# Kernel tuning notes

Hardware: AMD Instinct MI355X
Metric: run time of the kernel (lower is better)

Reference implementation:

```python
import jax, jax.numpy as jnp
import numpy as np

V, BLK, C, H, L = 50257, 1024, 1024, 16, 4
B, T = 2, 1024
D = C // H
EPS = 1e-5

def _ln(x, w):
    mu = jnp.mean(x, axis=-1, keepdims=True)
    var = jnp.mean(jnp.square(x - mu), axis=-1, keepdims=True)
    return (x - mu) * jax.lax.rsqrt(var + EPS) * w

def setup_inputs() -> dict:
    key = jax.random.key(0)
    ks = jax.random.split(key, 9)
    s = 0.02
    return {
        'idx': jax.random.randint(ks[0], (B, T), 0, V),
        'wte': jax.random.normal(ks[1], (V, C), jnp.float32) * s,
        'wpe': jax.random.normal(ks[2], (BLK, C), jnp.float32) * s,
        'ln1_w': jnp.ones((L, C), jnp.float32),
        'attn_w': jax.random.normal(ks[3], (L, 3 * C, C), jnp.float32) * s,   # torch Linear [out,in]
        'attnproj_w': jax.random.normal(ks[4], (L, C, C), jnp.float32) * (s / np.sqrt(2 * L)),
        'ln2_w': jnp.ones((L, C), jnp.float32),
        'fc_w': jax.random.normal(ks[5], (L, 4 * C, C), jnp.float32) * s,
        'mlpproj_w': jax.random.normal(ks[6], (L, C, 4 * C), jnp.float32) * (s / np.sqrt(2 * L)),
        'lnf_w': jnp.ones((C,), jnp.float32),
        'head_w': jax.random.normal(ks[7], (V, C), jnp.float32) * s,
    }

def _block(x, ln1_w, attn_w, attnproj_w, ln2_w, fc_w, mlpproj_w):
    b, t, c = x.shape
    h = _ln(x, ln1_w)
    qkv = h @ attn_w.T                                  # [B,T,3C]
    q, k, v = jnp.split(qkv, 3, axis=-1)
    q = q.reshape(b, t, H, D).transpose(0, 2, 1, 3)      # [B,H,T,D]
    k = k.reshape(b, t, H, D).transpose(0, 2, 1, 3)
    v = v.reshape(b, t, H, D).transpose(0, 2, 1, 3)
    att = jnp.einsum('bhqd,bhkd->bhqk', q, k) * (1.0 / np.sqrt(D))
    causal = jnp.tril(jnp.ones((t, t), bool))
    att = jnp.where(causal, att, jnp.float32(-jnp.inf))
    p = jax.nn.softmax(att, axis=-1)
    y = jnp.einsum('bhqk,bhkd->bhqd', p, v)
    y = y.transpose(0, 2, 1, 3).reshape(b, t, c)
    y = y @ attnproj_w.T
    x = x + y
    m = _ln(x, ln2_w)
    m = jax.nn.relu(m @ fc_w.T) @ mlpproj_w.T
    return x + m

def reference(idx, wte, wpe, ln1_w, attn_w, attnproj_w, ln2_w, fc_w, mlpproj_w, lnf_w, head_w):
    t = idx.shape[1]
    x = wte[idx] + wpe[:t]                               # [B,T,C]
    for i in range(L):
        x = _block(x, ln1_w[i], attn_w[i], attnproj_w[i], ln2_w[i], fc_w[i], mlpproj_w[i])
    x = _ln(x, lnf_w)
    return x @ head_w.T                                  # logits [B,T,V]
```

## Files before the change

### kernel.cpp

```cpp
#include <hip/hip_runtime.h>

typedef __bf16 bf16x8 __attribute__((ext_vector_type(8)));
typedef float f32x4 __attribute__((ext_vector_type(4)));
typedef unsigned short u16x8 __attribute__((ext_vector_type(8)));

#define LOG2E 1.4426950408889634f

__device__ __forceinline__ unsigned short f2bf(float f) {
  union { float f; unsigned u; } v; v.f = f;
  return (unsigned short)((v.u + 0x7fffu + ((v.u >> 16) & 1u)) >> 16);
}

__device__ __forceinline__ void gload16(const void* g, void* l) {
  __builtin_amdgcn_global_load_lds(
      (const __attribute__((address_space(1))) unsigned int*)g,
      (__attribute__((address_space(3))) unsigned int*)l, 16, 0, 0);
}

__global__ __launch_bounds__(256) void cvt_kernel(
    const float* __restrict__ s, unsigned short* __restrict__ d, int n8) {
  int i = blockIdx.x * 256 + threadIdx.x;
  int stride = gridDim.x * 256;
  for (; i < n8; i += stride) {
    float4 a = ((const float4*)s)[2 * i];
    float4 b = ((const float4*)s)[2 * i + 1];
    u16x8 o;
    o[0] = f2bf(a.x); o[1] = f2bf(a.y); o[2] = f2bf(a.z); o[3] = f2bf(a.w);
    o[4] = f2bf(b.x); o[5] = f2bf(b.y); o[6] = f2bf(b.z); o[7] = f2bf(b.w);
    ((u16x8*)d)[i] = o;
  }
}

__global__ __launch_bounds__(256) void embed_kernel(
    const int* __restrict__ idx, const float* __restrict__ wte,
    const float* __restrict__ wpe, float* __restrict__ x) {
  int row = blockIdx.x;
  int tok = idx[row];
  int t = row & 1023;
  float4 a = ((const float4*)(wte + (size_t)tok * 1024))[threadIdx.x];
  float4 p = ((const float4*)(wpe + (size_t)t * 1024))[threadIdx.x];
  a.x += p.x; a.y += p.y; a.z += p.z; a.w += p.w;
  ((float4*)(x + (size_t)row * 1024))[threadIdx.x] = a;
}

__global__ __launch_bounds__(256) void ln_kernel(
    const float* __restrict__ x, const float* __restrict__ w,
    unsigned short* __restrict__ out) {
  __shared__ float2 red[4];
  int row = blockIdx.x, tid = threadIdx.x;
  float4 v = ((const float4*)(x + (size_t)row * 1024))[tid];
  float s  = v.x + v.y + v.z + v.w;
  float s2 = v.x * v.x + v.y * v.y + v.z * v.z + v.w * v.w;
#pragma unroll
  for (int m = 32; m >= 1; m >>= 1) {
    s  += __shfl_xor(s, m, 64);
    s2 += __shfl_xor(s2, m, 64);
  }
  if ((tid & 63) == 0) red[tid >> 6] = make_float2(s, s2);
  __syncthreads();
  float S = 0.f, S2 = 0.f;
#pragma unroll
  for (int i = 0; i < 4; ++i) { S += red[i].x; S2 += red[i].y; }
  float mu = S * (1.f / 1024.f);
  float var = S2 * (1.f / 1024.f) - mu * mu;
  float rs = rsqrtf(var + 1e-5f);
  float4 wv = ((const float4*)w)[tid];
  ushort4 o;
  o.x = f2bf((v.x - mu) * rs * wv.x);
  o.y = f2bf((v.y - mu) * rs * wv.y);
  o.z = f2bf((v.z - mu) * rs * wv.z);
  o.w = f2bf((v.w - mu) * rs * wv.w);
  ((ushort4*)(out + (size_t)row * 1024))[tid] = o;
}

template <int MODE, bool WB16>
__global__ __launch_bounds__(256, 2) void gemm_bt(
    const unsigned short* __restrict__ A, const void* __restrict__ Wp,
    void* __restrict__ outp, const float* __restrict__ resid,
    unsigned short* __restrict__ qo, unsigned short* __restrict__ ko,
    unsigned short* __restrict__ vo, int M, int N, int K) {
  __shared__ unsigned short As[2][128 * 64];
  __shared__ unsigned short Bs[2][128 * 64];

  const int tid = threadIdx.x;
  const int lane = tid & 63;
  const int wv = tid >> 6;
  const int lr = lane & 15, lh = lane >> 4;
  const int nbm = M >> 7;
  const int nb = gridDim.x;
  const int bid = blockIdx.x;
  const int swz = (bid & 7) * (nb >> 3) + (bid >> 3);
  const int m0 = (swz % nbm) << 7;
  const int n0 = (swz / nbm) << 7;
  const int wm = (wv >> 1) << 6;
  const int wn = (wv & 1) << 6;
  const int nK = K >> 6;

  float4 breg[8];
  const float* Wf = (const float*)Wp;
  const unsigned short* Wb = (const unsigned short*)Wp;

  auto loadB = [&](int kt) {
#pragma unroll
    for (int j = 0; j < 8; ++j) {
      int u = j * 256 + tid;
      int rn = n0 + (u >> 4);
      if (rn >= N) rn = N - 1;
      breg[j] = *(const float4*)(Wf + (size_t)rn * K + kt * 64 + (u & 15) * 4);
    }
  };
  auto writeB = [&](int buf) {
#pragma unroll
    for (int j = 0; j < 8; ++j) {
      int u = j * 256 + tid;
      int row = u >> 4, q = u & 15;
      ushort4 h4;
      h4.x = f2bf(breg[j].x); h4.y = f2bf(breg[j].y);
      h4.z = f2bf(breg[j].z); h4.w = f2bf(breg[j].w);
      int off = row * 128 + ((q * 8) ^ ((row & 7) << 4));
      *(ushort4*)((char*)(&Bs[buf][0]) + off) = h4;
    }
  };
  auto stageA = [&](int buf, int kt) {
    const unsigned short* base = A + (size_t)m0 * K + kt * 64;
#pragma unroll
    for (int j = 0; j < 4; ++j) {
      int u = j * 256 + tid;
      int row = u >> 3, un = u & 7;
      gload16(base + (size_t)row * K + ((un ^ (row & 7)) << 3),
              (char*)(&As[buf][0]) + u * 16);
    }
  };
  auto stageB16 = [&](int buf, int kt) {
#pragma unroll
    for (int j = 0; j < 4; ++j) {
      int u = j * 256 + tid;
      int row = u >> 3, un = u & 7;
      size_t grow = (size_t)(n0 + row);
      if constexpr (MODE == 4) { if ((int)grow >= N) grow = N - 1; }
      gload16(Wb + grow * K + kt * 64 + ((un ^ (row & 7)) << 3),
              (char*)(&Bs[buf][0]) + u * 16);
    }
  };

  f32x4 acc[4][4];
#pragma unroll
  for (int a = 0; a < 4; ++a)
#pragma unroll
    for (int b = 0; b < 4; ++b) acc[a][b] = f32x4{0.f, 0.f, 0.f, 0.f};

  if constexpr (WB16) {
    stageA(0, 0);
    stageB16(0, 0);
  } else {
    loadB(0);
    stageA(0, 0);
    writeB(0);
  }
  __syncthreads();

  for (int kt = 0; kt < nK; ++kt) {
    int cur = kt & 1;
    if constexpr (WB16) {
      if (kt + 1 < nK) { stageA(cur ^ 1, kt + 1); stageB16(cur ^ 1, kt + 1); }
    } else {
      if (kt + 1 < nK) { loadB(kt + 1); stageA(cur ^ 1, kt + 1); }
    }

    bf16x8 af[4][2], bf[4][2];
#pragma unroll
    for (int mi = 0; mi < 4; ++mi)
#pragma unroll
      for (int ks = 0; ks < 2; ++ks) {
        int row = wm + mi * 16 + lr;
        int off = row * 128 + ((ks * 64 + lh * 16) ^ ((row & 7) << 4));
        af[mi][ks] = *(const bf16x8*)((const char*)(&As[cur][0]) + off);
      }
#pragma unroll
    for (int ni = 0; ni < 4; ++ni)
#pragma unroll
      for (int ks = 0; ks < 2; ++ks) {
        int row = wn + ni * 16 + lr;
        int off = row * 128 + ((ks * 64 + lh * 16) ^ ((row & 7) << 4));
        bf[ni][ks] = *(const bf16x8*)((const char*)(&Bs[cur][0]) + off);
      }
#pragma unroll
    for (int ks = 0; ks < 2; ++ks)
#pragma unroll
      for (int mi = 0; mi < 4; ++mi)
#pragma unroll
        for (int ni = 0; ni < 4; ++ni)
          acc[mi][ni] = __builtin_amdgcn_mfma_f32_16x16x32_bf16(
              af[mi][ks], bf[ni][ks], acc[mi][ni], 0, 0, 0);

    if constexpr (!WB16) {
      if (kt + 1 < nK) writeB(cur ^ 1);
    }
    __syncthreads();
  }

#pragma unroll
  for (int mi = 0; mi < 4; ++mi)
#pragma unroll
    for (int ni = 0; ni < 4; ++ni)
#pragma unroll
      for (int r = 0; r < 4; ++r) {
        int grow = m0 + wm + mi * 16 + lh * 4 + r;
        int gcol = n0 + wn + ni * 16 + lr;
        float val = acc[mi][ni][r];
        if constexpr (MODE == 1) val = fmaxf(val, 0.f);
        if constexpr (MODE == 0 || MODE == 1) {
          ((unsigned short*)outp)[(size_t)grow * N + gcol] = f2bf(val);
        } else if constexpr (MODE == 2) {
          ((float*)outp)[(size_t)grow * N + gcol] =
              resid[(size_t)grow * N + gcol] + val;
        } else if constexpr (MODE == 3) {
          int which = gcol >> 10, hh = (gcol >> 6) & 15, dd = gcol & 63;
          int b = grow >> 10, t = grow & 1023;
          unsigned short hv = f2bf(val);
          size_t bh = (size_t)(b * 16 + hh) << 16;
          if (which == 0)      qo[bh + t * 64 + dd] = hv;
          else if (which == 1) ko[bh + t * 64 + dd] = hv;
          else                 vo[bh + dd * 1024 + t] = hv;
        } else {
          if (gcol < N)
            ((float*)outp)[(size_t)grow * (size_t)N + gcol] = val;
        }
      }
}

__global__ __launch_bounds__(512, 2) void gemm256_bt(
    const unsigned short* __restrict__ A, const unsigned short* __restrict__ Wb,
    float* __restrict__ out, int M, int N, int K) {
  __shared__ unsigned short As[4][256 * 32];
  __shared__ unsigned short Bs[4][256 * 32];

  const int tid = threadIdx.x;
  const int lane = tid & 63;
  const int wv = tid >> 6;
  const int lr = lane & 15, lh = lane >> 4;
  const int wm = (wv >> 2) * 128;
  const int wn = (wv & 3) * 64;
  const int nbm = M >> 8;
  const int nb = gridDim.x;
  const int bid = blockIdx.x;
  const int swz = (bid & 7) * (nb >> 3) + (bid >> 3);
  const int m0 = (swz % nbm) << 8;
  const int n0 = (swz / nbm) << 8;
  const int nK = K >> 5;

  size_t aoff[2], boff[2];
  int ldst[2];
#pragma unroll
  for (int j = 0; j < 2; ++j) {
    int u = j * 512 + tid;
    int p = u >> 3, s = u & 7;
    int ss = s ^ (p & 7);
    int arow = m0 + 2 * p + (ss >> 2);
    int brow = n0 + 2 * p + (ss >> 2);
    if (brow >= N) brow = N - 1;
    aoff[j] = (size_t)arow * K + (ss & 3) * 8;
    boff[j] = (size_t)brow * K + (ss & 3) * 8;
    ldst[j] = u * 16;
  }

  auto stage = [&](int buf, int k) {
#pragma unroll
    for (int j = 0; j < 2; ++j)
      gload16(A + aoff[j] + k * 32, (char*)(&As[buf][0]) + ldst[j]);
#pragma unroll
    for (int j = 0; j < 2; ++j)
      gload16(Wb + boff[j] + k * 32, (char*)(&Bs[buf][0]) + ldst[j]);
  };

  f32x4 acc[8][4];
#pragma unroll
  for (int a = 0; a < 8; ++a)
#pragma unroll
    for (int b = 0; b < 4; ++b) acc[a][b] = f32x4{0.f, 0.f, 0.f, 0.f};

  stage(0, 0);
  if (nK > 1) stage(1, 1);
  if (nK > 2) stage(2, 2);
  if (nK > 2) asm volatile("s_waitcnt vmcnt(8)" ::: "memory");
  else        asm volatile("s_waitcnt vmcnt(0)" ::: "memory");
  __builtin_amdgcn_s_barrier();
  __builtin_amdgcn_sched_barrier(0);

  for (int k = 0; k < nK; ++k) {
    const int buf = k & 3;
    bf16x8 af[8], bfr[4];
#pragma unroll
    for (int ni = 0; ni < 4; ++ni) {
      int r = wn + ni * 16 + lr;
      int p = r >> 1;
      int off = p * 128 + (((((r & 1) << 2) | lh) ^ (p & 7)) << 4);
      bfr[ni] = *(const bf16x8*)((const char*)(&Bs[buf][0]) + off);
    }
#pragma unroll
    for (int mi = 0; mi < 8; ++mi) {
      int r = wm + mi * 16 + lr;
      int p = r >> 1;
      int off = p * 128 + (((((r & 1) << 2) | lh) ^ (p & 7)) << 4);
      af[mi] = *(const bf16x8*)((const char*)(&As[buf][0]) + off);
    }
    if (k + 3 < nK) stage((k + 3) & 3, k + 3);

    __builtin_amdgcn_s_setprio(1);
#pragma unroll
    for (int mi = 0; mi < 8; ++mi)
#pragma unroll
      for (int ni = 0; ni < 4; ++ni)
        acc[mi][ni] = __builtin_amdgcn_mfma_f32_16x16x32_bf16(
            af[mi], bfr[ni], acc[mi][ni], 0, 0, 0);
    __builtin_amdgcn_s_setprio(0);

    if (k + 1 < nK) {
      if (k + 4 <= nK)      asm volatile("s_waitcnt vmcnt(8)" ::: "memory");
      else if (k + 3 <= nK) asm volatile("s_waitcnt vmcnt(4)" ::: "memory");
      else                  asm volatile("s_waitcnt vmcnt(0)" ::: "memory");
      __builtin_amdgcn_s_barrier();
      __builtin_amdgcn_sched_barrier(0);
    }
  }

#pragma unroll
  for (int mi = 0; mi < 8; ++mi)
#pragma unroll
    for (int ni = 0; ni < 4; ++ni)
#pragma unroll
      for (int r = 0; r < 4; ++r) {
        int grow = m0 + wm + mi * 16 + lh * 4 + r;
        int gcol = n0 + wn + ni * 16 + lr;
        if (gcol < N) out[(size_t)grow * (size_t)N + gcol] = acc[mi][ni][r];
      }
}

__global__ __launch_bounds__(256, 2) void attn_kernel(
    const unsigned short* __restrict__ qb, const unsigned short* __restrict__ kb,
    const unsigned short* __restrict__ vt, unsigned short* __restrict__ yb) {
  __shared__ unsigned short Ks[2][64 * 64];
  __shared__ unsigned short Vs[2][64 * 64];
  __shared__ unsigned short Ps[4][32 * 64];

  const int tid = threadIdx.x, lane = tid & 63, wv = tid >> 6;
  const int lr = lane & 15, lh = lane >> 4;
  const int bid = blockIdx.x;
  const int bh = bid >> 3, qt = bid & 7;
  const int q0 = qt << 7;
  const unsigned short* qp = qb + ((size_t)bh << 16);
  const unsigned short* kp = kb + ((size_t)bh << 16);
  const unsigned short* vp = vt + ((size_t)bh << 16);

  bf16x8 qf[2][2];
#pragma unroll
  for (int mi = 0; mi < 2; ++mi)
#pragma unroll
    for (int ks = 0; ks < 2; ++ks) {
      int row = q0 + wv * 32 + mi * 16 + lr;
      qf[mi][ks] = *(const bf16x8*)(qp + (size_t)row * 64 + ks * 32 + lh * 8);
    }

  f32x4 o[2][4];
  float mr[2][4], lsum[2][4];
#pragma unroll
  for (int mi = 0; mi < 2; ++mi) {
#pragma unroll
    for (int di = 0; di < 4; ++di) o[mi][di] = f32x4{0.f, 0.f, 0.f, 0.f};
#pragma unroll
    for (int r = 0; r < 4; ++r) { mr[mi][r] = -1e30f; lsum[mi][r] = 0.f; }
  }

  const int wqmax = q0 + wv * 32 + 31;
  const int ntiles = (q0 + 128) >> 6;

  auto stageKV = [&](int buf, int t) {
    int kv0 = t << 6;
#pragma unroll
    for (int j = 0; j < 2; ++j) {
      int u = j * 256 + tid;
      int row = u >> 3, un = u & 7;
      gload16(kp + (size_t)(kv0 + row) * 64 + ((un ^ (row & 7)) << 3),
              (char*)(&Ks[buf][0]) + u * 16);
      gload16(vp + (size_t)row * 1024 + kv0 + ((un ^ (row & 7)) << 3),
              (char*)(&Vs[buf][0]) + u * 16);
    }
  };

  stageKV(0, 0);

  for (int t = 0; t < ntiles; ++t) {
    __syncthreads();
    if (t + 1 < ntiles) stageKV((t + 1) & 1, t + 1);
    int cur = t & 1;
    int kv0 = t << 6;
    if (kv0 <= wqmax) {
      f32x4 s[2][4];
#pragma unroll
      for (int mi = 0; mi < 2; ++mi)
#pragma unroll
        for (int ni = 0; ni < 4; ++ni) s[mi][ni] = f32x4{0.f, 0.f, 0.f, 0.f};

      bf16x8 kf[4][2];
#pragma unroll
      for (int ni = 0; ni < 4; ++ni)
#pragma unroll
        for (int ks = 0; ks < 2; ++ks) {
          int row = ni * 16 + lr;
          int off = row * 128 + ((ks * 64 + lh * 16) ^ ((row & 7) << 4));
          kf[ni][ks] = *(const bf16x8*)((const char*)(&Ks[cur][0]) + off);
        }
#pragma unroll
      for (int ks = 0; ks < 2; ++ks)
#pragma unroll
        for (int mi = 0; mi < 2; ++mi)
#pragma unroll
          for (int ni = 0; ni < 4; ++ni)
            s[mi][ni] = __builtin_amdgcn_mfma_f32_16x16x32_bf16(
                qf[mi][ks], kf[ni][ks], s[mi][ni], 0, 0, 0);

#pragma unroll
      for (int mi = 0; mi < 2; ++mi)
#pragma unroll
        for (int r = 0; r < 4; ++r) {
          int rowq = q0 + wv * 32 + mi * 16 + lh * 4 + r;
          float xv[4];
          float pm = -1e30f;
#pragma unroll
          for (int ni = 0; ni < 4; ++ni) {
            int col = kv0 + ni * 16 + lr;
            float xx = s[mi][ni][r] * 0.125f;
            if (col > rowq) xx = -1e30f;
            xv[ni] = xx;
            pm = fmaxf(pm, xx);
          }
#pragma unroll
          for (int msk = 1; msk < 16; msk <<= 1)
            pm = fmaxf(pm, __shfl_xor(pm, msk, 64));
          float mnew = fmaxf(mr[mi][r], pm);
          float al = exp2f((mr[mi][r] - mnew) * LOG2E);
          mr[mi][r] = mnew;
          float ps = 0.f;
#pragma unroll
          for (int ni = 0; ni < 4; ++ni) {
            float p = exp2f((xv[ni] - mnew) * LOG2E);
            s[mi][ni][r] = p;
            ps += p;
          }
#pragma unroll
          for (int msk = 1; msk < 16; msk <<= 1) ps += __shfl_xor(ps, msk, 64);
          lsum[mi][r] = lsum[mi][r] * al + ps;
#pragma unroll
          for (int di = 0; di < 4; ++di) o[mi][di][r] *= al;
        }

#pragma unroll
      for (int mi = 0; mi < 2; ++mi)
#pragma unroll
        for (int ni = 0; ni < 4; ++ni)
#pragma unroll
          for (int r = 0; r < 4; ++r) {
            int row = mi * 16 + lh * 4 + r;
            int off = row * 128 + (((ni * 16 + lr) * 2) ^ ((row & 7) << 4));
            *(unsigned short*)((char*)(&Ps[wv][0]) + off) = f2bf(s[mi][ni][r]);
          }

      bf16x8 pf[2][2], vf[4][2];
#pragma unroll
      for (int mi = 0; mi < 2; ++mi)
#pragma unroll
        for (int ks = 0; ks < 2; ++ks) {
          int row = mi * 16 + lr;
          int off = row * 128 + ((ks * 64 + lh * 16) ^ ((row & 7) << 4));
          pf[mi][ks] = *(const bf16x8*)((const char*)(&Ps[wv][0]) + off);
        }
#pragma unroll
      for (int di = 0; di < 4; ++di)
#pragma unroll
        for (int ks = 0; ks < 2; ++ks) {
          int row = di * 16 + lr;
          int off = row * 128 + ((ks * 64 + lh * 16) ^ ((row & 7) << 4));
          vf[di][ks] = *(const bf16x8*)((const char*)(&Vs[cur][0]) + off);
        }
#pragma unroll
      for (int ks = 0; ks < 2; ++ks)
#pragma unroll
        for (int mi = 0; mi < 2; ++mi)
#pragma unroll
          for (int di = 0; di < 4; ++di)
            o[mi][di] = __builtin_amdgcn_mfma_f32_16x16x32_bf16(
                pf[mi][ks], vf[di][ks], o[mi][di], 0, 0, 0);
    }
  }

  int b = bh >> 4, hh = bh & 15;
#pragma unroll
  for (int mi = 0; mi < 2; ++mi)
#pragma unroll
    for (int r = 0; r < 4; ++r) {
      float inv = 1.f / lsum[mi][r];
      int rowq = q0 + wv * 32 + mi * 16 + lh * 4 + r;
      size_t mg = (size_t)(b * 1024 + rowq) * 1024 + hh * 64;
#pragma unroll
      for (int di = 0; di < 4; ++di)
        yb[mg + di * 16 + lr] = f2bf(o[mi][di][r] * inv);
    }
}

extern "C" void kernel_launch(void* const* d_in, const int* in_sizes, int n_in,
                              void* d_out, int out_size, void* d_ws,
                              size_t ws_size, hipStream_t stream) {
  const int*   idx  = (const int*)d_in[0];
  const float* wte  = (const float*)d_in[1];
  const float* wpe  = (const float*)d_in[2];
  const float* ln1w = (const float*)d_in[3];
  const float* attnw= (const float*)d_in[4];
  const float* aprj = (const float*)d_in[5];
  const float* ln2w = (const float*)d_in[6];
  const float* fcw  = (const float*)d_in[7];
  const float* mprj = (const float*)d_in[8];
  const float* lnfw = (const float*)d_in[9];
  const float* hw   = (const float*)d_in[10];
  float* out = (float*)d_out;
  char* ws = (char*)d_ws;

  float* x            = (float*)ws;
  unsigned short* h   = (unsigned short*)(ws + ((size_t)8 << 20));
  unsigned short* qbf = (unsigned short*)(ws + ((size_t)12 << 20));
  unsigned short* kbf = (unsigned short*)(ws + ((size_t)16 << 20));
  unsigned short* vtb = (unsigned short*)(ws + ((size_t)20 << 20));
  unsigned short* ybf = (unsigned short*)(ws + ((size_t)24 << 20));
  unsigned short* mhb = (unsigned short*)(ws + ((size_t)12 << 20));

  size_t off = (size_t)28 << 20;
  unsigned short* attnw16 = (unsigned short*)(ws + off); off += (size_t)4 * 3072 * 1024 * 2;
  unsigned short* aprj16  = (unsigned short*)(ws + off); off += (size_t)4 * 1024 * 1024 * 2;
  unsigned short* fcw16   = (unsigned short*)(ws + off); off += (size_t)4 * 4096 * 1024 * 2;
  unsigned short* mprj16  = (unsigned short*)(ws + off); off += (size_t)4 * 1024 * 4096 * 2;
  unsigned short* hw16    = (unsigned short*)(ws + off); off += (size_t)50257 * 1024 * 2;
  const bool b16 = ws_size >= off;

  embed_kernel<<<2048, 256, 0, stream>>>(idx, wte, wpe, x);

  if (b16) {
    cvt_kernel<<<2048, 256, 0, stream>>>(attnw, attnw16, 4 * 3072 * 1024 / 8);
    cvt_kernel<<<2048, 256, 0, stream>>>(aprj,  aprj16,  4 * 1024 * 1024 / 8);
    cvt_kernel<<<2048, 256, 0, stream>>>(fcw,   fcw16,   4 * 4096 * 1024 / 8);
    cvt_kernel<<<2048, 256, 0, stream>>>(mprj,  mprj16,  4 * 1024 * 4096 / 8);
    cvt_kernel<<<2048, 256, 0, stream>>>(hw,    hw16,    50257 * 1024 / 8);
  }

  for (int l = 0; l < 4; ++l) {
    ln_kernel<<<2048, 256, 0, stream>>>(x, ln1w + l * 1024, h);
    if (b16)
      gemm_bt<3, true><<<16 * 24, 256, 0, stream>>>(
          h, attnw16 + (size_t)l * 3072 * 1024, nullptr, nullptr, qbf, kbf,
          vtb, 2048, 3072, 1024);
    else
      gemm_bt<3, false><<<16 * 24, 256, 0, stream>>>(
          h, attnw + (size_t)l * 3072 * 1024, nullptr, nullptr, qbf, kbf, vtb,
          2048, 3072, 1024);
    attn_kernel<<<256, 256, 0, stream>>>(qbf, kbf, vtb, ybf);
    if (b16)
      gemm_bt<2, true><<<16 * 8, 256, 0, stream>>>(
          ybf, aprj16 + (size_t)l * 1024 * 1024, x, x, nullptr, nullptr,
          nullptr, 2048, 1024, 1024);
    else
      gemm_bt<2, false><<<16 * 8, 256, 0, stream>>>(
          ybf, aprj + (size_t)l * 1024 * 1024, x, x, nullptr, nullptr, nullptr,
          2048, 1024, 1024);
    ln_kernel<<<2048, 256, 0, stream>>>(x, ln2w + l * 1024, h);
    if (b16)
      gemm_bt<1, true><<<16 * 32, 256, 0, stream>>>(
          h, fcw16 + (size_t)l * 4096 * 1024, mhb, nullptr, nullptr, nullptr,
          nullptr, 2048, 4096, 1024);
    else
      gemm_bt<1, false><<<16 * 32, 256, 0, stream>>>(
          h, fcw + (size_t)l * 4096 * 1024, mhb, nullptr, nullptr, nullptr,
          nullptr, 2048, 4096, 1024);
    if (b16)
      gemm_bt<2, true><<<16 * 8, 256, 0, stream>>>(
          mhb, mprj16 + (size_t)l * 1024 * 4096, x, x, nullptr, nullptr,
          nullptr, 2048, 1024, 4096);
    else
      gemm_bt<2, false><<<16 * 8, 256, 0, stream>>>(
          mhb, mprj + (size_t)l * 1024 * 4096, x, x, nullptr, nullptr, nullptr,
          2048, 1024, 4096);
  }

  ln_kernel<<<2048, 256, 0, stream>>>(x, lnfw, h);
  if (b16)
    gemm256_bt<<<8 * 197, 512, 0, stream>>>(h, hw16, out, 2048, 50257, 1024);
  else
    gemm_bt<4, false><<<16 * 393, 256, 0, stream>>>(
        h, hw, out, nullptr, nullptr, nullptr, nullptr, 2048, 50257, 1024);
}
```

Measured before the change: 1.372 ms.

## Split GEMM K-step into two interleaved phases of A-fragment loads and MFMAs

```diff
diff --git a/kernel.cpp b/kernel.cpp
--- a/kernel.cpp
+++ b/kernel.cpp
@@ -264,10 +264,12 @@
     ldst[j] = u * 16;
   }
 
-  auto stage = [&](int buf, int k) {
+  auto stageA = [&](int buf, int k) {
 #pragma unroll
     for (int j = 0; j < 2; ++j)
       gload16(A + aoff[j] + k * 32, (char*)(&As[buf][0]) + ldst[j]);
+  };
+  auto stageB = [&](int buf, int k) {
 #pragma unroll
     for (int j = 0; j < 2; ++j)
       gload16(Wb + boff[j] + k * 32, (char*)(&Bs[buf][0]) + ldst[j]);
@@ -279,17 +281,19 @@
 #pragma unroll
     for (int b = 0; b < 4; ++b) acc[a][b] = f32x4{0.f, 0.f, 0.f, 0.f};
 
-  stage(0, 0);
-  if (nK > 1) stage(1, 1);
-  if (nK > 2) stage(2, 2);
-  if (nK > 2) asm volatile("s_waitcnt vmcnt(8)" ::: "memory");
-  else        asm volatile("s_waitcnt vmcnt(0)" ::: "memory");
+  stageA(0, 0); stageB(0, 0);
+  if (nK > 1) { stageA(1, 1); stageB(1, 1); }
+  if (nK > 2) { stageA(2, 2); stageB(2, 2); }
+  if (nK > 2)      asm volatile("s_waitcnt vmcnt(8)" ::: "memory");
+  else if (nK > 1) asm volatile("s_waitcnt vmcnt(4)" ::: "memory");
+  else             asm volatile("s_waitcnt vmcnt(0)" ::: "memory");
   __builtin_amdgcn_s_barrier();
   __builtin_amdgcn_sched_barrier(0);
 
-  for (int k = 0; k < nK; ++k) {
-    const int buf = k & 3;
-    bf16x8 af[8], bfr[4];
+  for (int kt = 0; kt < nK; ++kt) {
+    const int buf = kt & 3;
+
+    bf16x8 bfr[4], af[4];
 #pragma unroll
     for (int ni = 0; ni < 4; ++ni) {
       int r = wn + ni * 16 + lr;
@@ -298,26 +302,51 @@
       bfr[ni] = *(const bf16x8*)((const char*)(&Bs[buf][0]) + off);
     }
 #pragma unroll
-    for (int mi = 0; mi < 8; ++mi) {
+    for (int mi = 0; mi < 4; ++mi) {
       int r = wm + mi * 16 + lr;
       int p = r >> 1;
       int off = p * 128 + (((((r & 1) << 2) | lh) ^ (p & 7)) << 4);
       af[mi] = *(const bf16x8*)((const char*)(&As[buf][0]) + off);
     }
-    if (k + 3 < nK) stage((k + 3) & 3, k + 3);
+    if (kt + 3 < nK) stageA((kt + 3) & 3, kt + 3);
+    __builtin_amdgcn_sched_barrier(0);
+    __builtin_amdgcn_s_barrier();
 
     __builtin_amdgcn_s_setprio(1);
 #pragma unroll
-    for (int mi = 0; mi < 8; ++mi)
+    for (int mi = 0; mi < 4; ++mi)
 #pragma unroll
       for (int ni = 0; ni < 4; ++ni)
         acc[mi][ni] = __builtin_amdgcn_mfma_f32_16x16x32_bf16(
             af[mi], bfr[ni], acc[mi][ni], 0, 0, 0);
     __builtin_amdgcn_s_setprio(0);
-
-    if (k + 1 < nK) {
-      if (k + 4 <= nK)      asm volatile("s_waitcnt vmcnt(8)" ::: "memory");
-      else if (k + 3 <= nK) asm volatile("s_waitcnt vmcnt(4)" ::: "memory");
+    __builtin_amdgcn_s_barrier();
+    __builtin_amdgcn_sched_barrier(0);
+
+    bf16x8 af2[4];
+#pragma unroll
+    for (int mi = 0; mi < 4; ++mi) {
+      int r = wm + (mi + 4) * 16 + lr;
+      int p = r >> 1;
+      int off = p * 128 + (((((r & 1) << 2) | lh) ^ (p & 7)) << 4);
+      af2[mi] = *(const bf16x8*)((const char*)(&As[buf][0]) + off);
+    }
+    if (kt + 3 < nK) stageB((kt + 3) & 3, kt + 3);
+    __builtin_amdgcn_sched_barrier(0);
+    __builtin_amdgcn_s_barrier();
+
+    __builtin_amdgcn_s_setprio(1);
+#pragma unroll
+    for (int mi = 0; mi < 4; ++mi)
+#pragma unroll
+      for (int ni = 0; ni < 4; ++ni)
+        acc[mi + 4][ni] = __builtin_amdgcn_mfma_f32_16x16x32_bf16(
+            af2[mi], bfr[ni], acc[mi + 4][ni], 0, 0, 0);
+    __builtin_amdgcn_s_setprio(0);
+
+    if (kt + 1 < nK) {
+      if (kt + 3 < nK)      asm volatile("s_waitcnt vmcnt(8)" ::: "memory");
+      else if (kt + 2 < nK) asm volatile("s_waitcnt vmcnt(4)" ::: "memory");
       else                  asm volatile("s_waitcnt vmcnt(0)" ::: "memory");
       __builtin_amdgcn_s_barrier();
       __builtin_amdgcn_sched_barrier(0);
```

New measurement: 1.395 ms. About the same (+1.6%).

## Add 4-stage direct-to-LDS pipelined 128x128 GEMM for transformer block matmuls

Applied to the files above, without the earlier changes.

```diff
diff --git a/kernel.cpp b/kernel.cpp
--- a/kernel.cpp
+++ b/kernel.cpp
@@ -229,6 +229,135 @@
       }
 }
 
+template <int MODE>
+__global__ __launch_bounds__(256, 2) void gemm128_bt(
+    const unsigned short* __restrict__ A, const unsigned short* __restrict__ Wb,
+    void* __restrict__ outp, const float* __restrict__ resid,
+    unsigned short* __restrict__ qo, unsigned short* __restrict__ ko,
+    unsigned short* __restrict__ vo, int M, int N, int K) {
+  __shared__ unsigned short As[4][128 * 32];
+  __shared__ unsigned short Bs[4][128 * 32];
+
+  const int tid = threadIdx.x;
+  const int lane = tid & 63;
+  const int wv = tid >> 6;
+  const int lr = lane & 15, lh = lane >> 4;
+  const int nbm = M >> 7;
+  const int nb = gridDim.x;
+  const int bid = blockIdx.x;
+  const int swz = (bid & 7) * (nb >> 3) + (bid >> 3);
+  const int m0 = (swz % nbm) << 7;
+  const int n0 = (swz / nbm) << 7;
+  const int wm = (wv >> 1) << 6;
+  const int wn = (wv & 1) << 6;
+  const int nK = K >> 5;
+
+  size_t aoff[2], boff[2];
+  int ldst[2];
+#pragma unroll
+  for (int j = 0; j < 2; ++j) {
+    int u = j * 256 + tid;
+    int p = u >> 3, s = u & 7;
+    int ss = s ^ (p & 7);
+    int arow = m0 + 2 * p + (ss >> 2);
+    int brow = n0 + 2 * p + (ss >> 2);
+    if (brow >= N) brow = N - 1;
+    aoff[j] = (size_t)arow * K + (ss & 3) * 8;
+    boff[j] = (size_t)brow * K + (ss & 3) * 8;
+    ldst[j] = u * 16;
+  }
+
+  auto stage = [&](int buf, int k) {
+#pragma unroll
+    for (int j = 0; j < 2; ++j)
+      gload16(A + aoff[j] + k * 32, (char*)(&As[buf][0]) + ldst[j]);
+#pragma unroll
+    for (int j = 0; j < 2; ++j)
+      gload16(Wb + boff[j] + k * 32, (char*)(&Bs[buf][0]) + ldst[j]);
+  };
+
+  f32x4 acc[4][4];
+#pragma unroll
+  for (int a = 0; a < 4; ++a)
+#pragma unroll
+    for (int b = 0; b < 4; ++b) acc[a][b] = f32x4{0.f, 0.f, 0.f, 0.f};
+
+  stage(0, 0);
+  if (nK > 1) stage(1, 1);
+  if (nK > 2) stage(2, 2);
+  if (nK > 2)      asm volatile("s_waitcnt vmcnt(8)" ::: "memory");
+  else if (nK > 1) asm volatile("s_waitcnt vmcnt(4)" ::: "memory");
+  else             asm volatile("s_waitcnt vmcnt(0)" ::: "memory");
+  __builtin_amdgcn_s_barrier();
+  __builtin_amdgcn_sched_barrier(0);
+
+  for (int kt = 0; kt < nK; ++kt) {
+    const int buf = kt & 3;
+    bf16x8 af[4], bfr[4];
+#pragma unroll
+    for (int ni = 0; ni < 4; ++ni) {
+      int r = wn + ni * 16 + lr;
+      int p = r >> 1;
+      int off = p * 128 + (((((r & 1) << 2) | lh) ^ (p & 7)) << 4);
+      bfr[ni] = *(const bf16x8*)((const char*)(&Bs[buf][0]) + off);
+    }
+#pragma unroll
+    for (int mi = 0; mi < 4; ++mi) {
+      int r = wm + mi * 16 + lr;
+      int p = r >> 1;
+      int off = p * 128 + (((((r & 1) << 2) | lh) ^ (p & 7)) << 4);
+      af[mi] = *(const bf16x8*)((const char*)(&As[buf][0]) + off);
+    }
+    if (kt + 3 < nK) stage((kt + 3) & 3, kt + 3);
+
+    __builtin_amdgcn_s_setprio(1);
+#pragma unroll
+    for (int mi = 0; mi < 4; ++mi)
+#pragma unroll
+      for (int ni = 0; ni < 4; ++ni)
+        acc[mi][ni] = __builtin_amdgcn_mfma_f32_16x16x32_bf16(
+            af[mi], bfr[ni], acc[mi][ni], 0, 0, 0);
+    __builtin_amdgcn_s_setprio(0);
+
+    if (kt + 1 < nK) {
+      if (kt + 4 <= nK)      asm volatile("s_waitcnt vmcnt(8)" ::: "memory");
+      else if (kt + 3 <= nK) asm volatile("s_waitcnt vmcnt(4)" ::: "memory");
+      else                   asm volatile("s_waitcnt vmcnt(0)" ::: "memory");
+      __builtin_amdgcn_s_barrier();
+      __builtin_amdgcn_sched_barrier(0);
+    }
+  }
+
+#pragma unroll
+  for (int mi = 0; mi < 4; ++mi)
+#pragma unroll
+    for (int ni = 0; ni < 4; ++ni)
+#pragma unroll
+      for (int r = 0; r < 4; ++r) {
+        int grow = m0 + wm + mi * 16 + lh * 4 + r;
+        int gcol = n0 + wn + ni * 16 + lr;
+        float val = acc[mi][ni][r];
+        if constexpr (MODE == 1) val = fmaxf(val, 0.f);
+        if constexpr (MODE == 0 || MODE == 1) {
+          ((unsigned short*)outp)[(size_t)grow * N + gcol] = f2bf(val);
+        } else if constexpr (MODE == 2) {
+          ((float*)outp)[(size_t)grow * N + gcol] =
+              resid[(size_t)grow * N + gcol] + val;
+        } else if constexpr (MODE == 3) {
+          int which = gcol >> 10, hh = (gcol >> 6) & 15, dd = gcol & 63;
+          int b = grow >> 10, t = grow & 1023;
+          unsigned short hv = f2bf(val);
+          size_t bh = (size_t)(b * 16 + hh) << 16;
+          if (which == 0)      qo[bh + t * 64 + dd] = hv;
+          else if (which == 1) ko[bh + t * 64 + dd] = hv;
+          else                 vo[bh + dd * 1024 + t] = hv;
+        } else {
+          if (gcol < N)
+            ((float*)outp)[(size_t)grow * (size_t)N + gcol] = val;
+        }
+      }
+}
+
 __global__ __launch_bounds__(512, 2) void gemm256_bt(
     const unsigned short* __restrict__ A, const unsigned short* __restrict__ Wb,
     float* __restrict__ out, int M, int N, int K) {
@@ -553,7 +682,7 @@
   for (int l = 0; l < 4; ++l) {
     ln_kernel<<<2048, 256, 0, stream>>>(x, ln1w + l * 1024, h);
     if (b16)
-      gemm_bt<3, true><<<16 * 24, 256, 0, stream>>>(
+      gemm128_bt<3><<<16 * 24, 256, 0, stream>>>(
           h, attnw16 + (size_t)l * 3072 * 1024, nullptr, nullptr, qbf, kbf,
           vtb, 2048, 3072, 1024);
     else
@@ -562,7 +691,7 @@
           2048, 3072, 1024);
     attn_kernel<<<256, 256, 0, stream>>>(qbf, kbf, vtb, ybf);
     if (b16)
-      gemm_bt<2, true><<<16 * 8, 256, 0, stream>>>(
+      gemm128_bt<2><<<16 * 8, 256, 0, stream>>>(
           ybf, aprj16 + (size_t)l * 1024 * 1024, x, x, nullptr, nullptr,
           nullptr, 2048, 1024, 1024);
     else
@@ -571,7 +700,7 @@
           2048, 1024, 1024);
     ln_kernel<<<2048, 256, 0, stream>>>(x, ln2w + l * 1024, h);
     if (b16)
-      gemm_bt<1, true><<<16 * 32, 256, 0, stream>>>(
+      gemm128_bt<1><<<16 * 32, 256, 0, stream>>>(
           h, fcw16 + (size_t)l * 4096 * 1024, mhb, nullptr, nullptr, nullptr,
           nullptr, 2048, 4096, 1024);
     else
@@ -579,7 +708,7 @@
           h, fcw + (size_t)l * 4096 * 1024, mhb, nullptr, nullptr, nullptr,
           nullptr, 2048, 4096, 1024);
     if (b16)
-      gemm_bt<2, true><<<16 * 8, 256, 0, stream>>>(
+      gemm128_bt<2><<<16 * 8, 256, 0, stream>>>(
           mhb, mprj16 + (size_t)l * 1024 * 4096, x, x, nullptr, nullptr,
           nullptr, 2048, 1024, 4096);
     else
```

New measurement: 1.317 ms. 1.04x faster.
